# Kernel tuning notes

Measured on AMD Instinct MI355X. Metric: run time of the kernel, lower is better.

## Reference

```python
import jax, jax.numpy as jnp
import numpy as np


def setup_inputs() -> dict:
    key = jax.random.key(0)
    ks = jax.random.split(key, 7)
    B, S, D, KP = 16, 4096, 64, 256  # batch*heads, seq_len, head_dim, linformer proj dim
    Q = jax.random.normal(ks[0], (B, S, D), dtype=jnp.float32)
    K = jax.random.normal(ks[1], (B, S, D), dtype=jnp.float32)
    V = jax.random.normal(ks[2], (B, S, D), dtype=jnp.float32)
    E_w = jax.random.normal(ks[3], (KP, S), dtype=jnp.float32) / np.sqrt(S)
    E_b = jax.random.normal(ks[4], (KP,), dtype=jnp.float32) * 0.01
    F_w = jax.random.normal(ks[5], (KP, S), dtype=jnp.float32) / np.sqrt(S)
    F_b = jax.random.normal(ks[6], (KP,), dtype=jnp.float32) * 0.01
    return {"Q": Q, "K": K, "V": V, "E_w": E_w, "E_b": E_b, "F_w": F_w, "F_b": F_b}


def reference(Q, K, V, E_w, E_b, F_w, F_b):
    # Linformer head (mask=None path); dropout is identity at inference.
    dim_k = K.shape[-1]
    scale = 1.0 / jnp.sqrt(jnp.float32(dim_k))
    # K.permute(0,2,1) -> [B, d, S]; E projects seq axis S -> k: [B, d, k]
    Kp = jnp.einsum('bsd,ks->bdk', K, E_w) + E_b  # [B, d, k]
    # V.permute -> F -> permute back: [B, k, d]
    Vp = jnp.einsum('bsd,ks->bkd', V, F_w) + F_b[None, :, None]  # [B, k, d]
    scores = jnp.einsum('bsd,bdk->bsk', Q, Kp) * scale  # [B, S, k]
    attn = jax.nn.softmax(scores, axis=-1)
    out = jnp.einsum('bsk,bkd->bsd', attn, Vp)  # [B, S, d]
    return (out, attn)
```

## Files before the change

### kernel.cpp

```cpp
#include <hip/hip_runtime.h>


#define B_  16
#define S_  4096
#define D_  64
#define KP_ 256

typedef short v8s __attribute__((ext_vector_type(8)));
typedef float v4f __attribute__((ext_vector_type(4)));

__device__ __forceinline__ short f2bf(float x) {
    union { float f; unsigned u; } v; v.f = x;
    unsigned r = v.u + 0x7FFFu + ((v.u >> 16) & 1u);
    return (short)(r >> 16);
}
__device__ __forceinline__ float bf2f(short h) {
    union { float f; unsigned u; } v; v.u = ((unsigned)(unsigned short)h) << 16;
    return v.f;
}

__global__ __launch_bounds__(256)
void wcvt_kernel(const float* __restrict__ E_w, const float* __restrict__ F_w,
                 short* __restrict__ Whi, short* __restrict__ Wlo)
{
    const int p = blockIdx.y;
    const float* W = p ? F_w : E_w;
    const size_t i4 = (size_t)blockIdx.x * 256 + threadIdx.x;
    float4 v = ((const float4*)W)[i4];
    short4 h, lo;
    h.x = f2bf(v.x); lo.x = f2bf(v.x - bf2f(h.x));
    h.y = f2bf(v.y); lo.y = f2bf(v.y - bf2f(h.y));
    h.z = f2bf(v.z); lo.z = f2bf(v.z - bf2f(h.z));
    h.w = f2bf(v.w); lo.w = f2bf(v.w - bf2f(h.w));
    const int k  = (int)(i4 >> 10);
    const int s0 = (int)(i4 & 1023) << 2;
    const size_t fo = (((size_t)p * 16 + (k >> 4)) * 128 + (s0 >> 5)) * 512
                    + (size_t)(((k & 15) + ((s0 >> 3) & 3) * 16) * 8) + (s0 & 7);
    *(short4*)(Whi + fo) = h;
    *(short4*)(Wlo + fo) = lo;
}

__global__ __launch_bounds__(512, 2)
void proj_mfma_kernel(const float* __restrict__ Kg, const float* __restrict__ Vg,
                      const short* __restrict__ Whi, const short* __restrict__ Wlo,
                      float* __restrict__ PpartK, float* __restrict__ PpartV)
{
    const int sc = blockIdx.x;
    const int p  = blockIdx.y;
    const int b  = blockIdx.z;

    const float* src = (p ? Vg : Kg) + ((size_t)b * S_ + sc * 512) * D_;

    __shared__ __align__(16) short Af[2][2][4][512];

    const int t  = threadIdx.x;
    const int wv = t >> 6;
    const int l  = t & 63;
    const int k16 = wv * 2;

    const size_t wbase = ((size_t)p * 16 + k16) * 128 * 512 + (size_t)(sc * 16) * 512 + (size_t)l * 8;

    v4f acc[2][4];
#pragma unroll
    for (int i = 0; i < 2; ++i)
#pragma unroll
        for (int m = 0; m < 4; ++m) acc[i][m] = (v4f){0.f, 0.f, 0.f, 0.f};

    const bool do_stage = (t < 256);
    const int sd   = t & 63;
    const int soct = (t >> 6) & 3;
    const int smt  = sd >> 4;
    const int sfl  = (sd & 15) + soct * 16;

    v8s whA[2], wlA[2], whB[2], wlB[2];
#pragma unroll
    for (int i = 0; i < 2; ++i) {
        size_t o = wbase + (size_t)i * 65536;
        whA[i] = *(const v8s*)(Whi + o);
        wlA[i] = *(const v8s*)(Wlo + o);
    }

    float g[8];
    if (do_stage) {
        const float* sp = src + (size_t)(soct * 8) * D_ + sd;
#pragma unroll
        for (int j = 0; j < 8; ++j) g[j] = sp[(size_t)j * D_];
        v8s hi, lo;
#pragma unroll
        for (int j = 0; j < 8; ++j) { short h = f2bf(g[j]); hi[j] = h; lo[j] = f2bf(g[j] - bf2f(h)); }
        *(v8s*)&Af[0][0][smt][sfl * 8] = hi;
        *(v8s*)&Af[0][1][smt][sfl * 8] = lo;
    }
    __syncthreads();

    auto step = [&](int st, v8s (&whc)[2], v8s (&wlc)[2], v8s (&whn)[2], v8s (&wln)[2]) {
        const int cur = st & 1;
        if (st + 1 < 16) {
#pragma unroll
            for (int i = 0; i < 2; ++i) {
                size_t o = wbase + (size_t)i * 65536 + (size_t)(st + 1) * 512;
                whn[i] = *(const v8s*)(Whi + o);
                wln[i] = *(const v8s*)(Wlo + o);
            }
            if (do_stage) {
                const float* sp = src + (size_t)((st + 1) * 32 + soct * 8) * D_ + sd;
#pragma unroll
                for (int j = 0; j < 8; ++j) g[j] = sp[(size_t)j * D_];
            }
        }
        v8s sh[4], sl[4];
#pragma unroll
        for (int m = 0; m < 4; ++m) {
            sh[m] = *(const v8s*)&Af[cur][0][m][l * 8];
            sl[m] = *(const v8s*)&Af[cur][1][m][l * 8];
        }
        if (p == 0) {
#pragma unroll
            for (int i = 0; i < 2; ++i)
#pragma unroll
                for (int m = 0; m < 4; ++m) {
                    acc[i][m] = __builtin_amdgcn_mfma_f32_16x16x32_bf16(whc[i], sh[m], acc[i][m], 0, 0, 0);
                    acc[i][m] = __builtin_amdgcn_mfma_f32_16x16x32_bf16(whc[i], sl[m], acc[i][m], 0, 0, 0);
                    acc[i][m] = __builtin_amdgcn_mfma_f32_16x16x32_bf16(wlc[i], sh[m], acc[i][m], 0, 0, 0);
                }
        } else {
#pragma unroll
            for (int i = 0; i < 2; ++i)
#pragma unroll
                for (int m = 0; m < 4; ++m) {
                    acc[i][m] = __builtin_amdgcn_mfma_f32_16x16x32_bf16(sh[m], whc[i], acc[i][m], 0, 0, 0);
                    acc[i][m] = __builtin_amdgcn_mfma_f32_16x16x32_bf16(sl[m], whc[i], acc[i][m], 0, 0, 0);
                    acc[i][m] = __builtin_amdgcn_mfma_f32_16x16x32_bf16(sh[m], wlc[i], acc[i][m], 0, 0, 0);
                }
        }
        if (st + 1 < 16 && do_stage) {
            v8s hi, lo;
#pragma unroll
            for (int j = 0; j < 8; ++j) { short h = f2bf(g[j]); hi[j] = h; lo[j] = f2bf(g[j] - bf2f(h)); }
            *(v8s*)&Af[cur ^ 1][0][smt][sfl * 8] = hi;
            *(v8s*)&Af[cur ^ 1][1][smt][sfl * 8] = lo;
        }
        __syncthreads();
    };

    for (int st2 = 0; st2 < 16; st2 += 2) {
        step(st2,     whA, wlA, whB, wlB);
        step(st2 + 1, whB, wlB, whA, wlA);
    }

    const int krow0 = wv * 32;
    if (p == 0) {
        float* outp = PpartK + ((size_t)sc * B_ + b) * (KP_ * D_);
#pragma unroll
        for (int i = 0; i < 2; ++i)
#pragma unroll
            for (int m = 0; m < 4; ++m)
#pragma unroll
                for (int r = 0; r < 4; ++r) {
                    int k = krow0 + i * 16 + (l >> 4) * 4 + r;
                    int d = m * 16 + (l & 15);
                    outp[(size_t)k * D_ + d] = acc[i][m][r];
                }
    } else {
        float* outp = PpartV + ((size_t)sc * B_ + b) * (KP_ * D_);
#pragma unroll
        for (int i = 0; i < 2; ++i)
#pragma unroll
            for (int m = 0; m < 4; ++m)
#pragma unroll
                for (int r = 0; r < 4; ++r) {
                    int d = m * 16 + (l >> 4) * 4 + r;
                    int k = krow0 + i * 16 + (l & 15);
                    outp[(size_t)d * KP_ + k] = acc[i][m][r];
                }
    }
}

__global__ __launch_bounds__(256)
void reduce_kernel(const float* __restrict__ PpartK, const float* __restrict__ PpartV,
                   const float* __restrict__ E_b, const float* __restrict__ F_b,
                   short* __restrict__ Kp_hi, short* __restrict__ Kp_lo,
                   short* __restrict__ Vp_hi)
{
    const int j    = blockIdx.x * 256 + threadIdx.x;
    const int side = j >> 16;
    const int i4   = j & 65535;
    const int flat = i4 * 4;
    const int b    = flat >> 14;
    const int dk   = flat & 16383;

    if (side == 0) {
        float4 a = make_float4(0.f, 0.f, 0.f, 0.f);
#pragma unroll
        for (int sc = 0; sc < 8; ++sc) {
            float4 v = *(const float4*)(PpartK + ((size_t)sc * B_ + b) * (KP_ * D_) + dk);
            a.x += v.x; a.y += v.y; a.z += v.z; a.w += v.w;
        }
        const int k = dk >> 6, d = dk & 63;
        float be = E_b[k];
        a.x += be; a.y += be; a.z += be; a.w += be;
        short4 h, lo;
        h.x = f2bf(a.x); lo.x = f2bf(a.x - bf2f(h.x));
        h.y = f2bf(a.y); lo.y = f2bf(a.y - bf2f(h.y));
        h.z = f2bf(a.z); lo.z = f2bf(a.z - bf2f(h.z));
        h.w = f2bf(a.w); lo.w = f2bf(a.w - bf2f(h.w));
        const size_t fo = (((size_t)b * 2 + (d >> 5)) * 16 + (k >> 4)) * 512
                        + (size_t)((k & 15) + ((d >> 3) & 3) * 16) * 8 + (d & 7);
        *(short4*)(Kp_hi + fo) = h;
        *(short4*)(Kp_lo + fo) = lo;
    } else {
        float4 a = make_float4(0.f, 0.f, 0.f, 0.f);
#pragma unroll
        for (int sc = 0; sc < 8; ++sc) {
            float4 v = *(const float4*)(PpartV + ((size_t)sc * B_ + b) * (KP_ * D_) + dk);
            a.x += v.x; a.y += v.y; a.z += v.z; a.w += v.w;
        }
        const int d = dk >> 8, k = dk & 255;
        float4 bf = *(const float4*)(F_b + k);
        a.x += bf.x; a.y += bf.y; a.z += bf.z; a.w += bf.w;
        short4 h;
        h.x = f2bf(a.x); h.y = f2bf(a.y); h.z = f2bf(a.z); h.w = f2bf(a.w);
        const size_t fo = (((size_t)b * 8 + (k >> 5)) * 4 + (d >> 4)) * 512
                        + (size_t)((d & 15) + ((k >> 3) & 3) * 16) * 8 + (k & 7);
        *(short4*)(Vp_hi + fo) = h;
    }
}

__global__ __launch_bounds__(256, 3)
void attn_mfma_kernel(const float* __restrict__ Qg,
                      const short* __restrict__ Kp_hi, const short* __restrict__ Kp_lo,
                      const short* __restrict__ Vp_hi,
                      float* __restrict__ attn_out, float* __restrict__ outg)
{
    const int st = blockIdx.x;
    const int b  = blockIdx.y;
    const int t  = threadIdx.x;
    const int wv = t >> 6;
    const int l  = t & 63;

    __shared__ __align__(16) short smem[64 * 264];
    __shared__ __align__(16) float Fst[4][4][264];
    short (*Qf)[2][4][512] = (short (*)[2][4][512])smem;
    short* Pl  = smem;
    short* KLl = smem + 8192;
    short* KLh = (short*)&Fst[0][0][0];

    {
        const int s    = t & 63;
        const int doct = t >> 6;
        const float* qrow = Qg + ((size_t)b * S_ + st * 64 + s) * D_;
        const int mt = s >> 4, fl = (s & 15) + doct * 16;
#pragma unroll
        for (int kd = 0; kd < 2; ++kd) {
            float4 v0 = *(const float4*)(qrow + kd * 32 + doct * 8);
            float4 v1 = *(const float4*)(qrow + kd * 32 + doct * 8 + 4);
            float gq[8] = {v0.x, v0.y, v0.z, v0.w, v1.x, v1.y, v1.z, v1.w};
            v8s hi, lo;
#pragma unroll
            for (int jj = 0; jj < 8; ++jj) { short h = f2bf(gq[jj]); hi[jj] = h; lo[jj] = f2bf(gq[jj] - bf2f(h)); }
            *(v8s*)&Qf[kd][0][mt][fl * 8] = hi;
            *(v8s*)&Qf[kd][1][mt][fl * 8] = lo;
        }
    }
    __syncthreads();

    v4f acc2[16];
#pragma unroll
    for (int nt = 0; nt < 16; ++nt) acc2[nt] = (v4f){0.f, 0.f, 0.f, 0.f};
#pragma unroll
    for (int kd = 0; kd < 2; ++kd) {
        {
            const size_t tbl = (((size_t)b * 2 + kd) * 16) * 512;
            const int4* gh = (const int4*)(Kp_hi + tbl);
            const int4* gl = (const int4*)(Kp_lo + tbl);
            int4* lh = (int4*)KLh;
            int4* ll = (int4*)KLl;
#pragma unroll
            for (int i = 0; i < 4; ++i) lh[t + i * 256] = gh[t + i * 256];
#pragma unroll
            for (int i = 0; i < 4; ++i) ll[t + i * 256] = gl[t + i * 256];
        }
        __syncthreads();
        v8s Ah = *(const v8s*)&Qf[kd][0][wv][l * 8];
        v8s Al = *(const v8s*)&Qf[kd][1][wv][l * 8];
#pragma unroll
        for (int nt = 0; nt < 16; ++nt) {
            v8s Bh = *(const v8s*)&KLh[nt * 512 + l * 8];
            v8s Bl = *(const v8s*)&KLl[nt * 512 + l * 8];
            acc2[nt] = __builtin_amdgcn_mfma_f32_16x16x32_bf16(Ah, Bh, acc2[nt], 0, 0, 0);
            acc2[nt] = __builtin_amdgcn_mfma_f32_16x16x32_bf16(Al, Bh, acc2[nt], 0, 0, 0);
            acc2[nt] = __builtin_amdgcn_mfma_f32_16x16x32_bf16(Ah, Bl, acc2[nt], 0, 0, 0);
        }
        __syncthreads();
    }

    const float scale = 0.125f;
    float* attn_b = attn_out + ((size_t)b * S_ + st * 64) * KP_;
    const int g = l >> 4;
#pragma unroll
    for (int r = 0; r < 4; ++r) {
        float m = -3.4e38f;
#pragma unroll
        for (int nt = 0; nt < 16; ++nt) m = fmaxf(m, acc2[nt][r]);
        m = fmaxf(m, __shfl_xor(m, 1));
        m = fmaxf(m, __shfl_xor(m, 2));
        m = fmaxf(m, __shfl_xor(m, 4));
        m = fmaxf(m, __shfl_xor(m, 8));
        float sum = 0.f;
#pragma unroll
        for (int nt = 0; nt < 16; ++nt) {
            float e = __expf((acc2[nt][r] - m) * scale);
            acc2[nt][r] = e; sum += e;
        }
        sum += __shfl_xor(sum, 1);
        sum += __shfl_xor(sum, 2);
        sum += __shfl_xor(sum, 4);
        sum += __shfl_xor(sum, 8);
        const float inv = 1.f / sum;
        const int s_loc = wv * 16 + g * 4 + r;
#pragma unroll
        for (int nt = 0; nt < 16; ++nt) {
            float pv = acc2[nt][r] * inv;
            Fst[wv][g][nt * 16 + (l & 15)] = pv;
            Pl[s_loc * 264 + nt * 16 + (l & 15)] = f2bf(pv);
        }
#pragma unroll
        for (int gg = 0; gg < 4; ++gg) {
            float4 vv = *(const float4*)&Fst[wv][gg][l * 4];
            *(float4*)(attn_b + (size_t)(wv * 16 + gg * 4 + r) * KP_ + l * 4) = vv;
        }
    }
    __syncthreads();
    {
        const int4* gv = (const int4*)(Vp_hi + (size_t)b * 16384);
        int4* lv = (int4*)KLh;
#pragma unroll
        for (int i = 0; i < 4; ++i) lv[t + i * 256] = gv[t + i * 256];
    }
    __syncthreads();
    v4f acc3[4];
#pragma unroll
    for (int nt = 0; nt < 4; ++nt) acc3[nt] = (v4f){0.f, 0.f, 0.f, 0.f};
#pragma unroll
    for (int kc = 0; kc < 4; ++kc) {
        v8s A3 = *(const v8s*)&Pl[(wv * 16 + (l & 15)) * 264 + kc * 32 + (l >> 4) * 8];
#pragma unroll
        for (int nt = 0; nt < 4; ++nt) {
            v8s B3 = *(const v8s*)&KLh[(kc * 4 + nt) * 512 + l * 8];
            acc3[nt] = __builtin_amdgcn_mfma_f32_16x16x32_bf16(A3, B3, acc3[nt], 0, 0, 0);
        }
    }
    __syncthreads();
    {
        const int4* gv = (const int4*)(Vp_hi + (size_t)b * 16384 + 8192);
        int4* lv = (int4*)KLh;
#pragma unroll
        for (int i = 0; i < 4; ++i) lv[t + i * 256] = gv[t + i * 256];
    }
    __syncthreads();
#pragma unroll
    for (int kc = 4; kc < 8; ++kc) {
        v8s A3 = *(const v8s*)&Pl[(wv * 16 + (l & 15)) * 264 + kc * 32 + (l >> 4) * 8];
#pragma unroll
        for (int nt = 0; nt < 4; ++nt) {
            v8s B3 = *(const v8s*)&KLh[((kc - 4) * 4 + nt) * 512 + l * 8];
            acc3[nt] = __builtin_amdgcn_mfma_f32_16x16x32_bf16(A3, B3, acc3[nt], 0, 0, 0);
        }
    }
    float* out_b = outg + ((size_t)b * S_ + st * 64) * D_;
#pragma unroll
    for (int nt = 0; nt < 4; ++nt)
#pragma unroll
        for (int r = 0; r < 4; ++r) {
            int s_loc = wv * 16 + (l >> 4) * 4 + r;
            out_b[(size_t)s_loc * D_ + nt * 16 + (l & 15)] = acc3[nt][r];
        }
}

extern "C" void kernel_launch(void* const* d_in, const int* in_sizes, int n_in,
                              void* d_out, int out_size, void* d_ws, size_t ws_size,
                              hipStream_t stream) {
    const float* Q   = (const float*)d_in[0];
    const float* K   = (const float*)d_in[1];
    const float* V   = (const float*)d_in[2];
    const float* E_w = (const float*)d_in[3];
    const float* E_b = (const float*)d_in[4];
    const float* F_w = (const float*)d_in[5];
    const float* F_b = (const float*)d_in[6];

    float* out  = (float*)d_out;
    float* attn = out + (size_t)B_ * S_ * D_;

    short* Whi   = (short*)d_ws;
    short* Wlo   = Whi + (size_t)2 * KP_ * S_;
    short* Kp_hi = Wlo + (size_t)2 * KP_ * S_;
    short* Kp_lo = Kp_hi + (size_t)B_ * KP_ * D_;
    short* Vp_hi = Kp_lo + (size_t)B_ * KP_ * D_;

    float* PpartK = attn;
    float* PpartV = attn + (size_t)8 * B_ * KP_ * D_;

    wcvt_kernel<<<dim3(KP_ * S_ / 4 / 256, 2), 256, 0, stream>>>(E_w, F_w, Whi, Wlo);
    proj_mfma_kernel<<<dim3(8, 2, B_), 512, 0, stream>>>(K, V, Whi, Wlo, PpartK, PpartV);
    reduce_kernel<<<dim3(512), 256, 0, stream>>>(PpartK, PpartV, E_b, F_b, Kp_hi, Kp_lo, Vp_hi);
    attn_mfma_kernel<<<dim3(S_ / 64, B_), 256, 0, stream>>>(Q, Kp_hi, Kp_lo, Vp_hi, attn, out);
}
```

Before: 181.2 us.

## Split projection over 16 sequence chunks and prefetch Vp into registers

The projection kernel now splits the sequence into 16 chunks of 256 instead of 8 chunks of 512, doubling the grid to 512 blocks. It raises the launch-bounds occupancy hint to 4 and replaces the register double-buffered weight prefetch with a plain in-loop load. The reduce kernel now sums 16 partials instead of 8. The attention kernel loads the Vp halves into registers early so the global latency overlaps the softmax and MFMA work. In exchange there are more partial buffers to write and reduce, and weight loads are no longer prefetched.

```diff
diff --git a/kernel.cpp b/kernel.cpp
--- a/kernel.cpp
+++ b/kernel.cpp
@@ -40,7 +40,7 @@
     *(short4*)(Wlo + fo) = lo;
 }
 
-__global__ __launch_bounds__(512, 2)
+__global__ __launch_bounds__(512, 4)
 void proj_mfma_kernel(const float* __restrict__ Kg, const float* __restrict__ Vg,
                       const short* __restrict__ Whi, const short* __restrict__ Wlo,
                       float* __restrict__ PpartK, float* __restrict__ PpartV)
@@ -49,7 +49,7 @@
     const int p  = blockIdx.y;
     const int b  = blockIdx.z;
 
-    const float* src = (p ? Vg : Kg) + ((size_t)b * S_ + sc * 512) * D_;
+    const float* src = (p ? Vg : Kg) + ((size_t)b * S_ + sc * 256) * D_;
 
     __shared__ __align__(16) short Af[2][2][4][512];
 
@@ -58,7 +58,7 @@
     const int l  = t & 63;
     const int k16 = wv * 2;
 
-    const size_t wbase = ((size_t)p * 16 + k16) * 128 * 512 + (size_t)(sc * 16) * 512 + (size_t)l * 8;
+    const size_t wbase = (((size_t)p * 16 + k16) * 128 + sc * 8) * 512 + (size_t)l * 8;
 
     v4f acc[2][4];
 #pragma unroll
@@ -72,14 +72,6 @@
     const int smt  = sd >> 4;
     const int sfl  = (sd & 15) + soct * 16;
 
-    v8s whA[2], wlA[2], whB[2], wlB[2];
-#pragma unroll
-    for (int i = 0; i < 2; ++i) {
-        size_t o = wbase + (size_t)i * 65536;
-        whA[i] = *(const v8s*)(Whi + o);
-        wlA[i] = *(const v8s*)(Wlo + o);
-    }
-
     float g[8];
     if (do_stage) {
         const float* sp = src + (size_t)(soct * 8) * D_ + sd;
@@ -93,20 +85,19 @@
     }
     __syncthreads();
 
-    auto step = [&](int st, v8s (&whc)[2], v8s (&wlc)[2], v8s (&whn)[2], v8s (&wln)[2]) {
+    for (int st = 0; st < 8; ++st) {
         const int cur = st & 1;
-        if (st + 1 < 16) {
-#pragma unroll
-            for (int i = 0; i < 2; ++i) {
-                size_t o = wbase + (size_t)i * 65536 + (size_t)(st + 1) * 512;
-                whn[i] = *(const v8s*)(Whi + o);
-                wln[i] = *(const v8s*)(Wlo + o);
-            }
-            if (do_stage) {
-                const float* sp = src + (size_t)((st + 1) * 32 + soct * 8) * D_ + sd;
-#pragma unroll
-                for (int j = 0; j < 8; ++j) g[j] = sp[(size_t)j * D_];
-            }
+        if (st + 1 < 8 && do_stage) {
+            const float* sp = src + (size_t)((st + 1) * 32 + soct * 8) * D_ + sd;
+#pragma unroll
+            for (int j = 0; j < 8; ++j) g[j] = sp[(size_t)j * D_];
+        }
+        v8s wh[2], wl2[2];
+#pragma unroll
+        for (int i = 0; i < 2; ++i) {
+            size_t o = wbase + (size_t)i * 65536 + (size_t)st * 512;
+            wh[i]  = *(const v8s*)(Whi + o);
+            wl2[i] = *(const v8s*)(Wlo + o);
         }
         v8s sh[4], sl[4];
 #pragma unroll
@@ -119,21 +110,21 @@
             for (int i = 0; i < 2; ++i)
 #pragma unroll
                 for (int m = 0; m < 4; ++m) {
-                    acc[i][m] = __builtin_amdgcn_mfma_f32_16x16x32_bf16(whc[i], sh[m], acc[i][m], 0, 0, 0);
-                    acc[i][m] = __builtin_amdgcn_mfma_f32_16x16x32_bf16(whc[i], sl[m], acc[i][m], 0, 0, 0);
-                    acc[i][m] = __builtin_amdgcn_mfma_f32_16x16x32_bf16(wlc[i], sh[m], acc[i][m], 0, 0, 0);
+                    acc[i][m] = __builtin_amdgcn_mfma_f32_16x16x32_bf16(wh[i],  sh[m], acc[i][m], 0, 0, 0);
+                    acc[i][m] = __builtin_amdgcn_mfma_f32_16x16x32_bf16(wh[i],  sl[m], acc[i][m], 0, 0, 0);
+                    acc[i][m] = __builtin_amdgcn_mfma_f32_16x16x32_bf16(wl2[i], sh[m], acc[i][m], 0, 0, 0);
                 }
         } else {
 #pragma unroll
             for (int i = 0; i < 2; ++i)
 #pragma unroll
                 for (int m = 0; m < 4; ++m) {
-                    acc[i][m] = __builtin_amdgcn_mfma_f32_16x16x32_bf16(sh[m], whc[i], acc[i][m], 0, 0, 0);
-                    acc[i][m] = __builtin_amdgcn_mfma_f32_16x16x32_bf16(sl[m], whc[i], acc[i][m], 0, 0, 0);
-                    acc[i][m] = __builtin_amdgcn_mfma_f32_16x16x32_bf16(sh[m], wlc[i], acc[i][m], 0, 0, 0);
+                    acc[i][m] = __builtin_amdgcn_mfma_f32_16x16x32_bf16(sh[m], wh[i],  acc[i][m], 0, 0, 0);
+                    acc[i][m] = __builtin_amdgcn_mfma_f32_16x16x32_bf16(sl[m], wh[i],  acc[i][m], 0, 0, 0);
+                    acc[i][m] = __builtin_amdgcn_mfma_f32_16x16x32_bf16(sh[m], wl2[i], acc[i][m], 0, 0, 0);
                 }
         }
-        if (st + 1 < 16 && do_stage) {
+        if (st + 1 < 8 && do_stage) {
             v8s hi, lo;
 #pragma unroll
             for (int j = 0; j < 8; ++j) { short h = f2bf(g[j]); hi[j] = h; lo[j] = f2bf(g[j] - bf2f(h)); }
@@ -141,11 +132,6 @@
             *(v8s*)&Af[cur ^ 1][1][smt][sfl * 8] = lo;
         }
         __syncthreads();
-    };
-
-    for (int st2 = 0; st2 < 16; st2 += 2) {
-        step(st2,     whA, wlA, whB, wlB);
-        step(st2 + 1, whB, wlB, whA, wlA);
     }
 
     const int krow0 = wv * 32;
@@ -192,7 +178,7 @@
     if (side == 0) {
         float4 a = make_float4(0.f, 0.f, 0.f, 0.f);
 #pragma unroll
-        for (int sc = 0; sc < 8; ++sc) {
+        for (int sc = 0; sc < 16; ++sc) {
             float4 v = *(const float4*)(PpartK + ((size_t)sc * B_ + b) * (KP_ * D_) + dk);
             a.x += v.x; a.y += v.y; a.z += v.z; a.w += v.w;
         }
@@ -211,7 +197,7 @@
     } else {
         float4 a = make_float4(0.f, 0.f, 0.f, 0.f);
 #pragma unroll
-        for (int sc = 0; sc < 8; ++sc) {
+        for (int sc = 0; sc < 16; ++sc) {
             float4 v = *(const float4*)(PpartV + ((size_t)sc * B_ + b) * (KP_ * D_) + dk);
             a.x += v.x; a.y += v.y; a.z += v.z; a.w += v.w;
         }
@@ -294,6 +280,13 @@
         __syncthreads();
     }
 
+    int4 vstg[4];
+    {
+        const int4* gv = (const int4*)(Vp_hi + (size_t)b * 16384);
+#pragma unroll
+        for (int i = 0; i < 4; ++i) vstg[i] = gv[t + i * 256];
+    }
+
     const float scale = 0.125f;
     float* attn_b = attn_out + ((size_t)b * S_ + st * 64) * KP_;
     const int g = l >> 4;
@@ -332,10 +325,14 @@
     }
     __syncthreads();
     {
-        const int4* gv = (const int4*)(Vp_hi + (size_t)b * 16384);
         int4* lv = (int4*)KLh;
 #pragma unroll
-        for (int i = 0; i < 4; ++i) lv[t + i * 256] = gv[t + i * 256];
+        for (int i = 0; i < 4; ++i) lv[t + i * 256] = vstg[i];
+    }
+    {
+        const int4* gv2 = (const int4*)(Vp_hi + (size_t)b * 16384 + 8192);
+#pragma unroll
+        for (int i = 0; i < 4; ++i) vstg[i] = gv2[t + i * 256];
     }
     __syncthreads();
     v4f acc3[4];
@@ -352,10 +349,9 @@
     }
     __syncthreads();
     {
-        const int4* gv = (const int4*)(Vp_hi + (size_t)b * 16384 + 8192);
         int4* lv = (int4*)KLh;
 #pragma unroll
-        for (int i = 0; i < 4; ++i) lv[t + i * 256] = gv[t + i * 256];
+        for (int i = 0; i < 4; ++i) lv[t + i * 256] = vstg[i];
     }
     __syncthreads();
 #pragma unroll
@@ -398,10 +394,10 @@
     short* Vp_hi = Kp_lo + (size_t)B_ * KP_ * D_;
 
     float* PpartK = attn;
-    float* PpartV = attn + (size_t)8 * B_ * KP_ * D_;
+    float* PpartV = attn + (size_t)16 * B_ * KP_ * D_;
 
     wcvt_kernel<<<dim3(KP_ * S_ / 4 / 256, 2), 256, 0, stream>>>(E_w, F_w, Whi, Wlo);
-    proj_mfma_kernel<<<dim3(8, 2, B_), 512, 0, stream>>>(K, V, Whi, Wlo, PpartK, PpartV);
+    proj_mfma_kernel<<<dim3(16, 2, B_), 512, 0, stream>>>(K, V, Whi, Wlo, PpartK, PpartV);
     reduce_kernel<<<dim3(512), 256, 0, stream>>>(PpartK, PpartV, E_b, F_b, Kp_hi, Kp_lo, Vp_hi);
     attn_mfma_kernel<<<dim3(S_ / 64, B_), 256, 0, stream>>>(Q, Kp_hi, Kp_lo, Vp_hi, attn, out);
 }
```

Measured after the change: 189.6 us. 4.6% more time.

## Prefetch Kp and Vp tiles into registers to overlap global loads with compute

Applied to the files above, without the earlier changes.

Issues the global loads for the first Kp hi/lo chunk before the Q conversion, and the second Kp hi chunk and both Vp chunks ahead of the compute stages that need them. Loads are held in registers and written to LDS after the current stage, which hides global-load latency behind MFMA and softmax work. The second Kp lo chunk is now read directly from global memory inside the MFMA loop rather than staged in LDS. This raises register pressure under launch_bounds(256,3) and could cause spills or lower occupancy.

```diff
diff --git a/kernel.cpp b/kernel.cpp
--- a/kernel.cpp
+++ b/kernel.cpp
@@ -243,7 +243,18 @@
     short (*Qf)[2][4][512] = (short (*)[2][4][512])smem;
     short* Pl  = smem;
     short* KLl = smem + 8192;
+    short* KH1 = smem;
     short* KLh = (short*)&Fst[0][0][0];
+
+    const size_t tb = (size_t)b * 16384;
+
+    int4 c0h[4], c0l[4];
+    {
+        const int4* gh = (const int4*)(Kp_hi + tb);
+        const int4* gl = (const int4*)(Kp_lo + tb);
+#pragma unroll
+        for (int i = 0; i < 4; ++i) { c0h[i] = gh[t + i * 256]; c0l[i] = gl[t + i * 256]; }
+    }
 
     {
         const int s    = t & 63;
@@ -262,36 +273,62 @@
             *(v8s*)&Qf[kd][1][mt][fl * 8] = lo;
         }
     }
-    __syncthreads();
+    {
+        int4* lh = (int4*)KLh; int4* ll = (int4*)KLl;
+#pragma unroll
+        for (int i = 0; i < 4; ++i) { lh[t + i * 256] = c0h[i]; ll[t + i * 256] = c0l[i]; }
+    }
+    __syncthreads();
+
+    v8s Ah0 = *(const v8s*)&Qf[0][0][wv][l * 8];
+    v8s Al0 = *(const v8s*)&Qf[0][1][wv][l * 8];
+    v8s Ah1 = *(const v8s*)&Qf[1][0][wv][l * 8];
+    v8s Al1 = *(const v8s*)&Qf[1][1][wv][l * 8];
+    __syncthreads();
+
+    int4 c1[4];
+    {
+        const int4* gh1 = (const int4*)(Kp_hi + tb + 8192);
+#pragma unroll
+        for (int i = 0; i < 4; ++i) c1[i] = gh1[t + i * 256];
+    }
 
     v4f acc2[16];
 #pragma unroll
     for (int nt = 0; nt < 16; ++nt) acc2[nt] = (v4f){0.f, 0.f, 0.f, 0.f};
 #pragma unroll
-    for (int kd = 0; kd < 2; ++kd) {
-        {
-            const size_t tbl = (((size_t)b * 2 + kd) * 16) * 512;
-            const int4* gh = (const int4*)(Kp_hi + tbl);
-            const int4* gl = (const int4*)(Kp_lo + tbl);
-            int4* lh = (int4*)KLh;
-            int4* ll = (int4*)KLl;
-#pragma unroll
-            for (int i = 0; i < 4; ++i) lh[t + i * 256] = gh[t + i * 256];
-#pragma unroll
-            for (int i = 0; i < 4; ++i) ll[t + i * 256] = gl[t + i * 256];
-        }
-        __syncthreads();
-        v8s Ah = *(const v8s*)&Qf[kd][0][wv][l * 8];
-        v8s Al = *(const v8s*)&Qf[kd][1][wv][l * 8];
+    for (int nt = 0; nt < 16; ++nt) {
+        v8s Bh = *(const v8s*)&KLh[nt * 512 + l * 8];
+        v8s Bl = *(const v8s*)&KLl[nt * 512 + l * 8];
+        acc2[nt] = __builtin_amdgcn_mfma_f32_16x16x32_bf16(Ah0, Bh, acc2[nt], 0, 0, 0);
+        acc2[nt] = __builtin_amdgcn_mfma_f32_16x16x32_bf16(Al0, Bh, acc2[nt], 0, 0, 0);
+        acc2[nt] = __builtin_amdgcn_mfma_f32_16x16x32_bf16(Ah0, Bl, acc2[nt], 0, 0, 0);
+    }
+    {
+        int4* lh1 = (int4*)KH1;
+#pragma unroll
+        for (int i = 0; i < 4; ++i) lh1[t + i * 256] = c1[i];
+    }
+    __syncthreads();
+
+    {
+        const short* gl1 = Kp_lo + tb + 8192;
 #pragma unroll
         for (int nt = 0; nt < 16; ++nt) {
-            v8s Bh = *(const v8s*)&KLh[nt * 512 + l * 8];
-            v8s Bl = *(const v8s*)&KLl[nt * 512 + l * 8];
-            acc2[nt] = __builtin_amdgcn_mfma_f32_16x16x32_bf16(Ah, Bh, acc2[nt], 0, 0, 0);
-            acc2[nt] = __builtin_amdgcn_mfma_f32_16x16x32_bf16(Al, Bh, acc2[nt], 0, 0, 0);
-            acc2[nt] = __builtin_amdgcn_mfma_f32_16x16x32_bf16(Ah, Bl, acc2[nt], 0, 0, 0);
-        }
-        __syncthreads();
+            v8s Bh = *(const v8s*)&KH1[nt * 512 + l * 8];
+            v8s Bl = *(const v8s*)(gl1 + (size_t)nt * 512 + (size_t)l * 8);
+            acc2[nt] = __builtin_amdgcn_mfma_f32_16x16x32_bf16(Ah1, Bh, acc2[nt], 0, 0, 0);
+            acc2[nt] = __builtin_amdgcn_mfma_f32_16x16x32_bf16(Al1, Bh, acc2[nt], 0, 0, 0);
+            acc2[nt] = __builtin_amdgcn_mfma_f32_16x16x32_bf16(Ah1, Bl, acc2[nt], 0, 0, 0);
+        }
+    }
+    __syncthreads();
+
+    int4 vstg[4];
+    {
+        const int4* gv = (const int4*)(Vp_hi + tb);
+#pragma unroll
+        for (int i = 0; i < 4; ++i) vstg[i] = gv[t + i * 256];
     }
 
     const float scale = 0.125f;
@@ -332,12 +369,16 @@
     }
     __syncthreads();
     {
-        const int4* gv = (const int4*)(Vp_hi + (size_t)b * 16384);
         int4* lv = (int4*)KLh;
 #pragma unroll
-        for (int i = 0; i < 4; ++i) lv[t + i * 256] = gv[t + i * 256];
-    }
-    __syncthreads();
+        for (int i = 0; i < 4; ++i) lv[t + i * 256] = vstg[i];
+    }
+    __syncthreads();
+    {
+        const int4* gv2 = (const int4*)(Vp_hi + tb + 8192);
+#pragma unroll
+        for (int i = 0; i < 4; ++i) vstg[i] = gv2[t + i * 256];
+    }
     v4f acc3[4];
 #pragma unroll
     for (int nt = 0; nt < 4; ++nt) acc3[nt] = (v4f){0.f, 0.f, 0.f, 0.f};
@@ -352,10 +393,9 @@
     }
     __syncthreads();
     {
-        const int4* gv = (const int4*)(Vp_hi + (size_t)b * 16384 + 8192);
         int4* lv = (int4*)KLh;
 #pragma unroll
-        for (int i = 0; i < 4; ++i) lv[t + i * 256] = gv[t + i * 256];
+        for (int i = 0; i < 4; ++i) lv[t + i * 256] = vstg[i];
     }
     __syncthreads();
 #pragma unroll
```

Result: slower. 190.4 us (+5.1%).
